# Performance work log

Hardware: AMD Instinct MI355X
Metric: run time of the kernel (lower is better)

## Reference

```python
import jax, jax.numpy as jnp
import numpy as np

N, E, IN, H, HEADS, L, OUT = 4096, 262144, 64, 128, 4, 2, 2
DH = H // HEADS  # 32, per-head dim for both GAT and global MHA
BN_EPS = 1e-5
NEG_SLOPE = 0.2  # GATConv leaky_relu default


def setup_inputs() -> dict:
    key = jax.random.key(0)
    ks = iter(jax.random.split(key, 32))
    rn = lambda shape, s: jax.random.normal(next(ks), shape, jnp.float32) * s
    return {
        "x": rn((N, IN), 1.0),
        "edge_index": jax.random.randint(next(ks), (2, E), 0, N),
        "w_in": rn((H, IN), IN ** -0.5),
        "b_in": rn((H,), 0.02),
        "w_gat": rn((L, H, H), H ** -0.5),
        "att_src": rn((L, HEADS, DH), 0.1),
        "att_dst": rn((L, HEADS, DH), 0.1),
        "b_gat": rn((L, H), 0.02),
        "w_qkv": rn((L, 3 * H, H), H ** -0.5),
        "b_qkv": rn((L, 3 * H), 0.02),
        "w_o": rn((L, H, H), H ** -0.5),
        "b_o": rn((L, H), 0.02),
        "bn_gamma": 1.0 + rn((L, 3, H), 0.05),
        "bn_beta": rn((L, 3, H), 0.05),
        "w1": rn((L, 2 * H, H), H ** -0.5),
        "b1": rn((L, 2 * H), 0.02),
        "w2": rn((L, H, 2 * H), (2 * H) ** -0.5),
        "b2": rn((L, H), 0.02),
        "w_out": rn((OUT, H), H ** -0.5),
        "b_out": rn((OUT,), 0.02),
    }


def _bn(h, g, b):
    # eval-mode BatchNorm1d with running_mean=0, running_var=1
    return h * (g / jnp.sqrt(1.0 + BN_EPS)) + b


def _gat(x, src, dst, w, a_src, a_dst, bias):
    # GATConv(hidden, hidden//heads, heads=HEADS, add_self_loops=False), concat=True
    xp = (x @ w.T).reshape(N, HEADS, DH)                  # [N, HEADS, DH]
    al_s = jnp.einsum('nhd,hd->nh', xp, a_src)            # [N, HEADS]
    al_d = jnp.einsum('nhd,hd->nh', xp, a_dst)
    logit = al_s[src] + al_d[dst]                         # [E, HEADS]
    logit = jnp.where(logit >= 0, logit, NEG_SLOPE * logit)
    m = jax.ops.segment_max(logit, dst, num_segments=N)   # scatter-softmax over dst
    m = jnp.where(jnp.isfinite(m), m, 0.0)
    e = jnp.exp(logit - m[dst])
    denom = jax.ops.segment_sum(e, dst, num_segments=N)
    alpha = e / (denom[dst] + 1e-16)
    out = jax.ops.segment_sum(alpha[:, :, None] * xp[src], dst, num_segments=N)
    return out.reshape(N, H) + bias


def _mha(x, wqkv, bqkv, wo, bo):
    # torch.nn.MultiheadAttention self-attention over all N nodes (one graph)
    qkv = x @ wqkv.T + bqkv
    q, k, v = jnp.split(qkv, 3, axis=-1)
    q = q.reshape(N, HEADS, DH)
    k = k.reshape(N, HEADS, DH)
    v = v.reshape(N, HEADS, DH)
    scores = jnp.einsum('nhd,mhd->hnm', q, k) / jnp.sqrt(jnp.float32(DH))
    attn = jax.nn.softmax(scores, axis=-1)
    out = jnp.einsum('hnm,mhd->nhd', attn, v).reshape(N, H)
    return out @ wo.T + bo


def reference(x, edge_index, w_in, b_in, w_gat, att_src, att_dst, b_gat,
              w_qkv, b_qkv, w_o, b_o, bn_gamma, bn_beta,
              w1, b1, w2, b2, w_out, b_out):
    src, dst = edge_index[0], edge_index[1]
    h = jax.nn.relu(x @ w_in.T + b_in)
    for l in range(L):
        # GPSConv: local GAT branch (dropout inactive in eval)
        h_loc = _gat(h, src, dst, w_gat[l], att_src[l], att_dst[l], b_gat[l]) + h
        h_loc = _bn(h_loc, bn_gamma[l, 0], bn_beta[l, 0])
        # GPSConv: global attention branch
        h_att = _mha(h, w_qkv[l], b_qkv[l], w_o[l], b_o[l]) + h
        h_att = _bn(h_att, bn_gamma[l, 1], bn_beta[l, 1])
        out = h_loc + h_att
        mlp = jax.nn.relu(out @ w1[l].T + b1[l]) @ w2[l].T + b2[l]
        out = _bn(out + mlp, bn_gamma[l, 2], bn_beta[l, 2])
        # GPSRiskModel residual + relu (dropout inactive in eval)
        h = jax.nn.relu(out + h)
    return h @ w_out.T + b_out
```

## Files before the change

kernel.cpp:

```cpp
#include <hip/hip_runtime.h>

#define NN 4096
#define EE 262144
#define INF_ 64
#define HH 128
#define HEADS 4
#define DH 32
#define LL 2
#define NH (NN * HH)
#define KSPLIT 16
#define L2E 1.4426950408889634f

typedef unsigned short u16;
typedef unsigned int u32;
using bf16x8 = __attribute__((ext_vector_type(8))) short;
using f32x4 = __attribute__((ext_vector_type(4))) float;

__device__ __forceinline__ float bf2f(u16 v) { return __uint_as_float(((u32)v) << 16); }
__device__ __forceinline__ u16 f2bf(float f) {
    u32 u = __float_as_uint(f);
    u32 r = (u + 0x7fffu + ((u >> 16) & 1u)) >> 16;
    return (u16)r;
}
__device__ __forceinline__ u32 encf(float f) {
    u32 b = __float_as_uint(f);
    return (b & 0x80000000u) ? ~b : (b | 0x80000000u);
}
__device__ __forceinline__ float decf(u32 u) {
    u32 b = (u & 0x80000000u) ? (u & 0x7fffffffu) : ~u;
    return __uint_as_float(b);
}

__global__ __launch_bounds__(256) void k_detect(const u16* __restrict__ x, int* __restrict__ flag,
                                                int* __restrict__ cnt, u32* __restrict__ gmax) {
    int t = threadIdx.x;
    for (int i = t; i < NN; i += 256) cnt[i] = 0;
    if (t < 16) gmax[t] = 0;
    __shared__ int cs[256];
    u16 v = x[2 * t];
    int e = (v >> 7) & 0xFF;
    cs[t] = (e >= 100 && e <= 140) ? 1 : 0;
    __syncthreads();
    for (int s = 128; s > 0; s >>= 1) {
        if (t < s) cs[t] += cs[t + s];
        __syncthreads();
    }
    if (t == 0) *flag = (cs[0] >= 128) ? 1 : 0;
}

#define MAXSEG 16
struct SegF { const void* src[MAXSEG]; int dst[MAXSEG]; int n[MAXSEG]; int cnt; };
struct SegB { const void* src[8]; u16* dst[8]; u16* dst2[8]; int n[8]; int cnt; };
__global__ __launch_bounds__(256) void k_prep(SegF SF, float* __restrict__ W, SegB SB,
                                              const int* __restrict__ flag,
                                              const int* __restrict__ dst, int* __restrict__ cnt) {
    int bid = blockIdx.x, t = threadIdx.x;
    if (bid < 96) {
        int seg = bid >> 3, bx = bid & 7;
        if (seg >= SF.cnt) return;
        int n = SF.n[seg];
        float* d = W + SF.dst[seg];
        const void* s = SF.src[seg];
        int f = *flag;
        for (int i = bx * 256 + t; i < n; i += 8 * 256)
            d[i] = f ? bf2f(((const u16*)s)[i]) : ((const float*)s)[i];
    } else if (bid < 992) {
        int b2 = bid - 96;
        int seg = b2 >> 7, bx = b2 & 127;
        if (seg >= SB.cnt) return;
        int f = *flag;
        u16* d = SB.dst[seg];
        u16* d2 = SB.dst2[seg];
        if (f && !d2) return;
        int n = SB.n[seg];
        const void* s = SB.src[seg];
        for (int i = bx * 256 + t; i < n; i += 128 * 256) {
            if (d2) {
                float v = f ? bf2f(((const u16*)s)[i]) : ((const float*)s)[i];
                u16 h = f2bf(v);
                d[i] = h;
                d2[i] = f2bf(v - bf2f(h));
            } else {
                d[i] = f2bf(((const float*)s)[i]);
            }
        }
    } else {
        int e = (bid - 992) * 256 + t;
        if (e < EE) atomicAdd(&cnt[dst[e]], 1);
    }
}

__global__ __launch_bounds__(128) void k_mgemm(const u16* __restrict__ Ahi, const u16* __restrict__ Alo,
                                               const u16* __restrict__ Wc, const u16* __restrict__ Wd,
                                               const int* __restrict__ flag,
                                               const float* __restrict__ bias,
                                               float* __restrict__ outf, u16* __restrict__ outb16,
                                               u16* __restrict__ outhi, u16* __restrict__ outlo,
                                               int K, int J, int relu, int jtiles,
                                               const int* __restrict__ scnt, int* __restrict__ srowstart,
                                               int* __restrict__ scursor) {
    __shared__ int part[128];
    if ((int)blockIdx.y >= jtiles) {
        if (blockIdx.x != 0 || scnt == nullptr) return;
        int t = threadIdx.x;
        int loc[32];
        int s = 0;
#pragma unroll
        for (int i = 0; i < 32; ++i) { loc[i] = s; s += scnt[t * 32 + i]; }
        part[t] = s;
        __syncthreads();
        for (int off = 1; off < 128; off <<= 1) {
            int v = part[t];
            int a = (t >= off) ? part[t - off] : 0;
            __syncthreads();
            part[t] = v + a;
            __syncthreads();
        }
        int base = (t == 0) ? 0 : part[t - 1];
#pragma unroll
        for (int i = 0; i < 32; ++i) {
            srowstart[t * 32 + i] = base + loc[i];
            scursor[t * 32 + i] = base + loc[i];
        }
        return;
    }
    const u16* Wb = (*flag) ? Wd : Wc;
    int wave = threadIdx.x >> 6, lane = threadIdx.x & 63;
    int grp = lane >> 4, lcol = lane & 15;
    int m0 = blockIdx.x * 32 + wave * 16;
    int j0 = blockIdx.y * 64;
    f32x4 acc[4];
#pragma unroll
    for (int s = 0; s < 4; ++s) acc[s] = (f32x4){0.f, 0.f, 0.f, 0.f};
    const u16* ah = Ahi + (size_t)(m0 + lcol) * K + grp * 8;
    const u16* al = Alo + (size_t)(m0 + lcol) * K + grp * 8;
    const u16* wb = Wb + (size_t)(j0 + lcol) * K + grp * 8;
    for (int k = 0; k < K; k += 32) {
        bf16x8 va = *(const bf16x8*)(ah + k);
        bf16x8 vl = *(const bf16x8*)(al + k);
#pragma unroll
        for (int s = 0; s < 4; ++s) {
            bf16x8 vw = *(const bf16x8*)(wb + (size_t)s * 16 * K + k);
            acc[s] = __builtin_amdgcn_mfma_f32_16x16x32_bf16(va, vw, acc[s], 0, 0, 0);
            acc[s] = __builtin_amdgcn_mfma_f32_16x16x32_bf16(vl, vw, acc[s], 0, 0, 0);
        }
    }
#pragma unroll
    for (int s = 0; s < 4; ++s) {
        int col = j0 + s * 16 + lcol;
        float bs = bias ? bias[col] : 0.f;
#pragma unroll
        for (int r = 0; r < 4; ++r) {
            float v = acc[s][r] + bs;
            if (relu) v = fmaxf(v, 0.f);
            size_t idx = (size_t)(m0 + grp * 4 + r) * J + col;
            if (outf) outf[idx] = v;
            if (outb16) outb16[idx] = f2bf(v);
            if (outhi) {
                u16 hv = f2bf(v);
                outhi[idx] = hv;
                outlo[idx] = f2bf(v - bf2f(hv));
            }
        }
    }
}

__global__ __launch_bounds__(128) void k_gemm_gq(const u16* __restrict__ Ahi, const u16* __restrict__ Alo,
                                                 const u16* __restrict__ wgatc, const u16* __restrict__ wgatd,
                                                 const u16* __restrict__ wqkvc, const u16* __restrict__ wqkvd,
                                                 const int* __restrict__ flag,
                                                 const float* __restrict__ bqkv,
                                                 u16* __restrict__ xpb, u16* __restrict__ qkvb,
                                                 const int* __restrict__ esrc_src, const int* __restrict__ esrc_dst,
                                                 int* __restrict__ cursor, int* __restrict__ esrc) {
    if (blockIdx.y >= 8) {
        int b = (blockIdx.y - 8) * 128 + blockIdx.x;
        for (int e = b * 128 + threadIdx.x; e < EE; e += 32768) {
            int d = esrc_dst[e];
            int p = atomicAdd(&cursor[d], 1);
            esrc[p] = esrc_src[e];
        }
        return;
    }
    int wave = threadIdx.x >> 6, lane = threadIdx.x & 63;
    int grp = lane >> 4, lcol = lane & 15;
    int m0 = blockIdx.x * 32 + wave * 16;
    int jb = blockIdx.y;
    int j0 = jb * 64;
    int f = *flag;
    const u16* wgat = f ? wgatd : wgatc;
    const u16* wqkv = f ? wqkvd : wqkvc;
    const u16* Wb = (jb < 2) ? (wgat + (size_t)j0 * HH) : (wqkv + (size_t)(j0 - 128) * HH);
    f32x4 acc[4];
#pragma unroll
    for (int s = 0; s < 4; ++s) acc[s] = (f32x4){0.f, 0.f, 0.f, 0.f};
    const u16* ah = Ahi + (size_t)(m0 + lcol) * HH + grp * 8;
    const u16* al = Alo + (size_t)(m0 + lcol) * HH + grp * 8;
    const u16* wb = Wb + (size_t)lcol * HH + grp * 8;
    for (int k = 0; k < HH; k += 32) {
        bf16x8 va = *(const bf16x8*)(ah + k);
        bf16x8 vl = *(const bf16x8*)(al + k);
#pragma unroll
        for (int s = 0; s < 4; ++s) {
            bf16x8 vw = *(const bf16x8*)(wb + (size_t)s * 16 * HH + k);
            acc[s] = __builtin_amdgcn_mfma_f32_16x16x32_bf16(va, vw, acc[s], 0, 0, 0);
            acc[s] = __builtin_amdgcn_mfma_f32_16x16x32_bf16(vl, vw, acc[s], 0, 0, 0);
        }
    }
    if (jb < 2) {
#pragma unroll
        for (int s = 0; s < 4; ++s) {
            int col = j0 + s * 16 + lcol;
#pragma unroll
            for (int r = 0; r < 4; ++r)
                xpb[(size_t)(m0 + grp * 4 + r) * HH + col] = f2bf(acc[s][r]);
        }
    } else {
#pragma unroll
        for (int s = 0; s < 4; ++s) {
            int colq = j0 - 128 + s * 16 + lcol;
            float bs = bqkv[colq];
#pragma unroll
            for (int r = 0; r < 4; ++r)
                qkvb[(size_t)(m0 + grp * 4 + r) * 384 + colq] = f2bf(acc[s][r] + bs);
        }
    }
}

__global__ __launch_bounds__(128) void k_gemm_wo(const u16* __restrict__ Ahi, const u16* __restrict__ Alo,
                                                 const u16* __restrict__ Wc, const u16* __restrict__ Wd,
                                                 const int* __restrict__ flag,
                                                 const float* __restrict__ bias,
                                                 const float* __restrict__ gatb, const float* __restrict__ hbuf,
                                                 const float* __restrict__ bgat, const float* __restrict__ gam,
                                                 const float* __restrict__ bet,
                                                 float* __restrict__ outb, u16* __restrict__ ohi,
                                                 u16* __restrict__ olo) {
    const u16* Wb = (*flag) ? Wd : Wc;
    int wave = threadIdx.x >> 6, lane = threadIdx.x & 63;
    int grp = lane >> 4, lcol = lane & 15;
    int m0 = blockIdx.x * 32 + wave * 16;
    int j0 = blockIdx.y * 64;
    f32x4 acc[4];
#pragma unroll
    for (int s = 0; s < 4; ++s) acc[s] = (f32x4){0.f, 0.f, 0.f, 0.f};
    const u16* ah = Ahi + (size_t)(m0 + lcol) * HH + grp * 8;
    const u16* al = Alo + (size_t)(m0 + lcol) * HH + grp * 8;
    const u16* wb = Wb + (size_t)(j0 + lcol) * HH + grp * 8;
    for (int k = 0; k < HH; k += 32) {
        bf16x8 va = *(const bf16x8*)(ah + k);
        bf16x8 vl = *(const bf16x8*)(al + k);
#pragma unroll
        for (int s = 0; s < 4; ++s) {
            bf16x8 vw = *(const bf16x8*)(wb + (size_t)s * 16 * HH + k);
            acc[s] = __builtin_amdgcn_mfma_f32_16x16x32_bf16(va, vw, acc[s], 0, 0, 0);
            acc[s] = __builtin_amdgcn_mfma_f32_16x16x32_bf16(vl, vw, acc[s], 0, 0, 0);
        }
    }
    float rs = rsqrtf(1.00001f);
#pragma unroll
    for (int s = 0; s < 4; ++s) {
        int col = j0 + s * 16 + lcol;
        float bs = bias[col];
        float g0 = gam[col] * rs, b0 = bet[col];
        float g1 = gam[HH + col] * rs, b1 = bet[HH + col];
        float bg = bgat[col];
#pragma unroll
        for (int r = 0; r < 4; ++r) {
            size_t idx = (size_t)(m0 + grp * 4 + r) * HH + col;
            float proj = acc[s][r] + bs;
            float hv = hbuf[idx];
            float hl = g0 * (gatb[idx] + bg + hv) + b0;
            float ha = g1 * (proj + hv) + b1;
            float v = hl + ha;
            outb[idx] = v;
            u16 hb = f2bf(v);
            ohi[idx] = hb;
            olo[idx] = f2bf(v - bf2f(hb));
        }
    }
}

__global__ __launch_bounds__(128) void k_gemm_mlp(const u16* __restrict__ Ahi, const u16* __restrict__ Alo,
                                                  const u16* __restrict__ W1c, const u16* __restrict__ W1d,
                                                  const u16* __restrict__ W2c, const u16* __restrict__ W2d,
                                                  const int* __restrict__ flag,
                                                  const float* __restrict__ b1, const float* __restrict__ b2,
                                                  const float* __restrict__ outb, const float* __restrict__ gam2,
                                                  const float* __restrict__ bet2,
                                                  float* __restrict__ hbuf, u16* __restrict__ hhi,
                                                  u16* __restrict__ hlo) {
    __shared__ u16 Hhi[16][264];
    __shared__ u16 Hlo[16][264];
    int f = *flag;
    const u16* W1 = f ? W1d : W1c;
    const u16* W2 = f ? W2d : W2c;
    int wave = threadIdx.x >> 6, lane = threadIdx.x & 63;
    int grp = lane >> 4, lcol = lane & 15;
    int m0 = blockIdx.x * 16;
    const u16* ah = Ahi + (size_t)(m0 + lcol) * HH + grp * 8;
    const u16* al = Alo + (size_t)(m0 + lcol) * HH + grp * 8;
#pragma unroll
    for (int jt = 0; jt < 2; ++jt) {
        int j0 = wave * 128 + jt * 64;
        f32x4 acc[4];
#pragma unroll
        for (int s = 0; s < 4; ++s) acc[s] = (f32x4){0.f, 0.f, 0.f, 0.f};
        const u16* wb = W1 + (size_t)(j0 + lcol) * HH + grp * 8;
#pragma unroll
        for (int k = 0; k < HH; k += 32) {
            bf16x8 va = *(const bf16x8*)(ah + k);
            bf16x8 vl = *(const bf16x8*)(al + k);
#pragma unroll
            for (int s = 0; s < 4; ++s) {
                bf16x8 vw = *(const bf16x8*)(wb + (size_t)s * 16 * HH + k);
                acc[s] = __builtin_amdgcn_mfma_f32_16x16x32_bf16(va, vw, acc[s], 0, 0, 0);
                acc[s] = __builtin_amdgcn_mfma_f32_16x16x32_bf16(vl, vw, acc[s], 0, 0, 0);
            }
        }
#pragma unroll
        for (int s = 0; s < 4; ++s) {
            int col = j0 + s * 16 + lcol;
            float bs = b1[col];
#pragma unroll
            for (int r = 0; r < 4; ++r) {
                float v = fmaxf(acc[s][r] + bs, 0.f);
                int row = grp * 4 + r;
                u16 hv = f2bf(v);
                Hhi[row][col] = hv;
                Hlo[row][col] = f2bf(v - bf2f(hv));
            }
        }
    }
    __syncthreads();
    int j0 = wave * 64;
    f32x4 acc[4];
#pragma unroll
    for (int s = 0; s < 4; ++s) acc[s] = (f32x4){0.f, 0.f, 0.f, 0.f};
    const u16* wb = W2 + (size_t)(j0 + lcol) * 256 + grp * 8;
#pragma unroll
    for (int k = 0; k < 256; k += 32) {
        bf16x8 va = *(const bf16x8*)(&Hhi[lcol][k + grp * 8]);
        bf16x8 vl = *(const bf16x8*)(&Hlo[lcol][k + grp * 8]);
#pragma unroll
        for (int s = 0; s < 4; ++s) {
            bf16x8 vw = *(const bf16x8*)(wb + (size_t)s * 16 * 256 + k);
            acc[s] = __builtin_amdgcn_mfma_f32_16x16x32_bf16(va, vw, acc[s], 0, 0, 0);
            acc[s] = __builtin_amdgcn_mfma_f32_16x16x32_bf16(vl, vw, acc[s], 0, 0, 0);
        }
    }
    float rs = rsqrtf(1.00001f);
#pragma unroll
    for (int s = 0; s < 4; ++s) {
        int col = j0 + s * 16 + lcol;
        float bs = b2[col];
        float g2 = gam2[col] * rs, bb2 = bet2[col];
#pragma unroll
        for (int r = 0; r < 4; ++r) {
            size_t idx = (size_t)(m0 + grp * 4 + r) * HH + col;
            float mlpo = acc[s][r] + bs;
            float o2 = g2 * (outb[idx] + mlpo) + bb2;
            float v = fmaxf(o2 + hbuf[idx], 0.f);
            hbuf[idx] = v;
            u16 hb = f2bf(v);
            hhi[idx] = hb;
            hlo[idx] = f2bf(v - bf2f(hb));
        }
    }
}

__global__ __launch_bounds__(256) void k_splitlog(const u16* __restrict__ qkvb,
                                                  float* __restrict__ PM, float* __restrict__ PL,
                                                  u16* __restrict__ PO,
                                                  const u16* __restrict__ xpb,
                                                  const float* __restrict__ asrc,
                                                  const float* __restrict__ adst,
                                                  float* __restrict__ als, float* __restrict__ ald,
                                                  u32* __restrict__ gmax) {
    __shared__ __align__(16) u16 Klds[64][40];
    __shared__ __align__(16) u32 Vlds[32][40];
    __shared__ __align__(16) u16 Plds[4][32][36];

    if (blockIdx.x >= 2048) {
        float* red = (float*)&Klds[0][0];
        int t = (blockIdx.x - 2048) * 256 + threadIdx.x;
        int n = t >> 2, hh = t & 3;
        const u16* xr = xpb + (size_t)n * HH + hh * DH;
        float s1 = 0.f, s2 = 0.f;
#pragma unroll
        for (int d = 0; d < DH; ++d) {
            float v = bf2f(xr[d]);
            s1 += v * asrc[hh * DH + d];
            s2 += v * adst[hh * DH + d];
        }
        als[t] = s1;
        ald[t] = s2;
        int lt = threadIdx.x;
        red[lt] = s1;
        __syncthreads();
        for (int off = 128; off >= 4; off >>= 1) {
            if (lt < off) red[lt] = fmaxf(red[lt], red[lt + off]);
            __syncthreads();
        }
        if (lt < 4) atomicMax(&gmax[lt], encf(red[lt]));
        __syncthreads();
        red[lt] = s2;
        __syncthreads();
        for (int off = 128; off >= 4; off >>= 1) {
            if (lt < off) red[lt] = fmaxf(red[lt], red[lt + off]);
            __syncthreads();
        }
        if (lt < 4) atomicMax(&gmax[4 + lt], encf(red[lt]));
        return;
    }

    const float C1 = 0.17677669529663687f * L2E;
    int head = blockIdx.x & 3;
    int qt = (blockIdx.x >> 2) & 31;
    int ks = blockIdx.x >> 7;
    int tid = threadIdx.x;
    int wave = tid >> 6, lane = tid & 63;
    int grp = lane >> 4, lcol = lane & 15;

    int qrow0 = qt * 128 + wave * 32;
    bf16x8 aQ0 = *(const bf16x8*)(qkvb + (size_t)(qrow0 + lcol) * 384 + head * 32 + grp * 8);
    bf16x8 aQ1 = *(const bf16x8*)(qkvb + (size_t)(qrow0 + 16 + lcol) * 384 + head * 32 + grp * 8);

    short onev = (lcol == 0) ? (short)0x3F80 : (short)0;
    bf16x8 bOne = {onev, onev, onev, onev, onev, onev, onev, onev};

    f32x4 oc00 = {0.f, 0.f, 0.f, 0.f}, oc01 = {0.f, 0.f, 0.f, 0.f};
    f32x4 oc10 = {0.f, 0.f, 0.f, 0.f}, oc11 = {0.f, 0.f, 0.f, 0.f};
    f32x4 ol0 = {0.f, 0.f, 0.f, 0.f}, ol1 = {0.f, 0.f, 0.f, 0.f};
    float msh = -INFINITY;

    int isK = (tid < 128);
    int st = tid & 127;
    int skey = st >> 1, shalf = (st & 1) * 16;
    int vj = st & 15, vc = (st >> 4) & 1, dgrp = st >> 5;
    const u16* kptr = qkvb + 128 + head * 32 + shalf;
    const u16* vptr = qkvb + 256 + head * 32 + dgrp * 8;
    int vk0 = vc * 32 + vj;
    int vk1 = vc * 32 + 16 + vj;

    int kt0 = ks * (NN / KSPLIT);
    bf16x8 r0, r1;
    if (isK) {
        r0 = *(const bf16x8*)(kptr + (size_t)(kt0 + skey) * 384);
        r1 = *(const bf16x8*)(kptr + (size_t)(kt0 + skey) * 384 + 8);
    } else {
        r0 = *(const bf16x8*)(vptr + (size_t)(kt0 + vk0) * 384);
        r1 = *(const bf16x8*)(vptr + (size_t)(kt0 + vk1) * 384);
    }

    const int NT = (NN / KSPLIT) / 64;
    for (int t = 0; t < NT; ++t) {
        if (isK) {
            *(bf16x8*)(&Klds[skey][shalf]) = r0;
            *(bf16x8*)(&Klds[skey][shalf + 8]) = r1;
        } else {
#pragma unroll
            for (int j = 0; j < 8; ++j)
                Vlds[dgrp * 8 + j][vc * 20 + vj] = (u32)(u16)r0[j] | ((u32)(u16)r1[j] << 16);
        }
        __syncthreads();
        if (t + 1 < NT) {
            int kn = kt0 + (t + 1) * 64;
            if (isK) {
                r0 = *(const bf16x8*)(kptr + (size_t)(kn + skey) * 384);
                r1 = *(const bf16x8*)(kptr + (size_t)(kn + skey) * 384 + 8);
            } else {
                r0 = *(const bf16x8*)(vptr + (size_t)(kn + vk0) * 384);
                r1 = *(const bf16x8*)(vptr + (size_t)(kn + vk1) * 384);
            }
        }
        f32x4 sc0[4], sc1[4];
        f32x4 zero = {0.f, 0.f, 0.f, 0.f};
        __builtin_amdgcn_s_setprio(1);
#pragma unroll
        for (int s = 0; s < 4; ++s) {
            bf16x8 bK = *(const bf16x8*)(&Klds[s * 16 + lcol][grp * 8]);
            sc0[s] = __builtin_amdgcn_mfma_f32_16x16x32_bf16(aQ0, bK, zero, 0, 0, 0);
            sc1[s] = __builtin_amdgcn_mfma_f32_16x16x32_bf16(aQ1, bK, zero, 0, 0, 0);
        }
        __builtin_amdgcn_s_setprio(0);
        float mymax = sc0[0][0];
#pragma unroll
        for (int s = 0; s < 4; ++s)
#pragma unroll
            for (int r = 0; r < 4; ++r) {
                mymax = fmaxf(mymax, sc0[s][r]);
                mymax = fmaxf(mymax, sc1[s][r]);
            }
        mymax = fmaxf(mymax, __shfl_xor(mymax, 1));
        mymax = fmaxf(mymax, __shfl_xor(mymax, 2));
        mymax = fmaxf(mymax, __shfl_xor(mymax, 4));
        mymax = fmaxf(mymax, __shfl_xor(mymax, 8));
        float mnew = fmaxf(msh, mymax * C1);
        float cc = __builtin_exp2f(msh - mnew);
        msh = mnew;
        oc00 *= cc; oc01 *= cc; ol0 *= cc;
        oc10 *= cc; oc11 *= cc; ol1 *= cc;
#pragma unroll
        for (int c2 = 0; c2 < 2; ++c2) {
#pragma unroll
            for (int r = 0; r < 4; ++r) {
                float p0 = __builtin_exp2f(__builtin_fmaf(sc0[2 * c2][r], C1, -mnew));
                float p1 = __builtin_exp2f(__builtin_fmaf(sc0[2 * c2 + 1][r], C1, -mnew));
                *(u32*)(&Plds[wave][grp * 4 + r][2 * lcol]) =
                    __builtin_amdgcn_perm(__float_as_uint(p1), __float_as_uint(p0), 0x07060302u);
                float q0 = __builtin_exp2f(__builtin_fmaf(sc1[2 * c2][r], C1, -mnew));
                float q1 = __builtin_exp2f(__builtin_fmaf(sc1[2 * c2 + 1][r], C1, -mnew));
                *(u32*)(&Plds[wave][16 + grp * 4 + r][2 * lcol]) =
                    __builtin_amdgcn_perm(__float_as_uint(q1), __float_as_uint(q0), 0x07060302u);
            }
            bf16x8 aP0 = *(const bf16x8*)(&Plds[wave][lcol][grp * 8]);
            bf16x8 aP1 = *(const bf16x8*)(&Plds[wave][16 + lcol][grp * 8]);
            bf16x8 bV0 = *(const bf16x8*)(&Vlds[lcol][c2 * 20 + grp * 4]);
            bf16x8 bV1 = *(const bf16x8*)(&Vlds[16 + lcol][c2 * 20 + grp * 4]);
            __builtin_amdgcn_s_setprio(1);
            oc00 = __builtin_amdgcn_mfma_f32_16x16x32_bf16(aP0, bV0, oc00, 0, 0, 0);
            oc01 = __builtin_amdgcn_mfma_f32_16x16x32_bf16(aP0, bV1, oc01, 0, 0, 0);
            ol0 = __builtin_amdgcn_mfma_f32_16x16x32_bf16(aP0, bOne, ol0, 0, 0, 0);
            oc10 = __builtin_amdgcn_mfma_f32_16x16x32_bf16(aP1, bV0, oc10, 0, 0, 0);
            oc11 = __builtin_amdgcn_mfma_f32_16x16x32_bf16(aP1, bV1, oc11, 0, 0, 0);
            ol1 = __builtin_amdgcn_mfma_f32_16x16x32_bf16(aP1, bOne, ol1, 0, 0, 0);
            __builtin_amdgcn_s_setprio(0);
        }
        __syncthreads();
    }
#pragma unroll
    for (int r = 0; r < 4; ++r) {
        int row0 = qrow0 + grp * 4 + r;
        size_t b0 = ((size_t)row0 * HEADS + head) * KSPLIT + ks;
        PO[b0 * 32 + lcol] = f2bf(oc00[r]);
        PO[b0 * 32 + 16 + lcol] = f2bf(oc01[r]);
        int row1 = row0 + 16;
        size_t b1 = ((size_t)row1 * HEADS + head) * KSPLIT + ks;
        PO[b1 * 32 + lcol] = f2bf(oc10[r]);
        PO[b1 * 32 + 16 + lcol] = f2bf(oc11[r]);
        if (lcol == 0) {
            PM[b0] = msh;
            PL[b0] = ol0[r];
            PM[b1] = msh;
            PL[b1] = ol1[r];
        }
    }
}

#define GCHUNK 256
__global__ __launch_bounds__(128) void k_gatcomb(const int* __restrict__ esrc, const int* __restrict__ rowstart,
                                                 const int* __restrict__ cnt, const float* __restrict__ als,
                                                 const float* __restrict__ ald, const u16* __restrict__ xpb,
                                                 float* __restrict__ gatout, const u32* __restrict__ gmax,
                                                 const float* __restrict__ PM, const float* __restrict__ PL,
                                                 const u16* __restrict__ PO, u16* __restrict__ atthi,
                                                 u16* __restrict__ attlo) {
    __shared__ float red[512];
    __shared__ float elds[GCHUNK * 4];
    __shared__ int slds[GCHUNK];
    int t = threadIdx.x;

    if (blockIdx.x >= NN) {
        int n2 = blockIdx.x - NN;
        float* wn = red;
        if (t < 64) {
            int head = t >> 4, ks = t & 15;
            size_t b = ((size_t)n2 * HEADS + head) * KSPLIT + ks;
            float pm = PM[b];
            float m = pm;
#pragma unroll
            for (int off = 1; off < 16; off <<= 1) m = fmaxf(m, __shfl_xor(m, off));
            float w = __builtin_exp2f(pm - m);
            float lw = PL[b] * w;
#pragma unroll
            for (int off = 1; off < 16; off <<= 1) lw += __shfl_xor(lw, off);
            wn[t] = w / lw;
        }
        __syncthreads();
        int head = t >> 5, dim = t & 31;
        size_t b0 = ((size_t)n2 * HEADS + head) * KSPLIT;
        float o = 0.f;
#pragma unroll
        for (int k = 0; k < KSPLIT; ++k)
            o += wn[head * 16 + k] * bf2f(PO[(b0 + k) * 32 + dim]);
        size_t idx = (size_t)n2 * HH + t;
        u16 h = f2bf(o);
        atthi[idx] = h;
        attlo[idx] = f2bf(o - bf2f(h));
        return;
    }

    int n = blockIdx.x;
    int base = rowstart[n], c = cnt[n];
    float4 adv = ((const float4*)ald)[n];
    float ad[4] = {adv.x, adv.y, adv.z, adv.w};
    float M2[4];
#pragma unroll
    for (int h = 0; h < 4; ++h) {
        float bound = decf(gmax[h]) + decf(gmax[4 + h]);
        float M = bound >= 0.f ? bound : 0.2f * bound;
        M2[h] = M * L2E;
    }
    float dsum[4] = {0.f, 0.f, 0.f, 0.f};
    float acc = 0.f;
    int ht = t >> 5;
    for (int ch = 0; ch < c; ch += GCHUNK) {
        int cn = min(GCHUNK, c - ch);
        __syncthreads();
        for (int i = t; i < cn; i += 128) {
            int s = esrc[base + ch + i];
            slds[i] = s;
            float4 as = ((const float4*)als)[s];
            float lg, e;
            lg = as.x + ad[0]; lg = lg >= 0.f ? lg : 0.2f * lg; e = __builtin_exp2f(lg * L2E - M2[0]); elds[i * 4 + 0] = e; dsum[0] += e;
            lg = as.y + ad[1]; lg = lg >= 0.f ? lg : 0.2f * lg; e = __builtin_exp2f(lg * L2E - M2[1]); elds[i * 4 + 1] = e; dsum[1] += e;
            lg = as.z + ad[2]; lg = lg >= 0.f ? lg : 0.2f * lg; e = __builtin_exp2f(lg * L2E - M2[2]); elds[i * 4 + 2] = e; dsum[2] += e;
            lg = as.w + ad[3]; lg = lg >= 0.f ? lg : 0.2f * lg; e = __builtin_exp2f(lg * L2E - M2[3]); elds[i * 4 + 3] = e; dsum[3] += e;
        }
        __syncthreads();
        int i = 0;
        for (; i + 4 <= cn; i += 4) {
            int s0 = slds[i], s1 = slds[i + 1], s2 = slds[i + 2], s3 = slds[i + 3];
            float x0 = bf2f(xpb[(size_t)s0 * HH + t]);
            float x1 = bf2f(xpb[(size_t)s1 * HH + t]);
            float x2 = bf2f(xpb[(size_t)s2 * HH + t]);
            float x3 = bf2f(xpb[(size_t)s3 * HH + t]);
            acc += elds[i * 4 + ht] * x0 + elds[(i + 1) * 4 + ht] * x1;
            acc += elds[(i + 2) * 4 + ht] * x2 + elds[(i + 3) * 4 + ht] * x3;
        }
        for (; i < cn; ++i) acc += elds[i * 4 + ht] * bf2f(xpb[(size_t)slds[i] * HH + t]);
    }
    __syncthreads();
#pragma unroll
    for (int h = 0; h < 4; ++h) red[h * 128 + t] = dsum[h];
    __syncthreads();
    for (int s2 = 64; s2 > 0; s2 >>= 1) {
        if (t < s2) {
#pragma unroll
            for (int h = 0; h < 4; ++h)
                red[h * 128 + t] += red[h * 128 + t + s2];
        }
        __syncthreads();
    }
    float inv = 1.f / (red[ht * 128] + 1e-16f);
    gatout[(size_t)n * HH + t] = acc * inv;
}

__global__ __launch_bounds__(64) void k_out(const float* __restrict__ h, const float* __restrict__ w,
                                            const float* __restrict__ b, void* __restrict__ yout,
                                            const int* __restrict__ flag) {
    int n = blockIdx.x, l = threadIdx.x;
    float a0 = 0.f, a1 = 0.f;
    for (int k = l; k < HH; k += 64) {
        float hv = h[(size_t)n * HH + k];
        a0 += hv * w[k];
        a1 += hv * w[HH + k];
    }
#pragma unroll
    for (int off = 32; off > 0; off >>= 1) {
        a0 += __shfl_xor(a0, off);
        a1 += __shfl_xor(a1, off);
    }
    if (l == 0) {
        float o0 = a0 + b[0], o1 = a1 + b[1];
        if (*flag) {
            u16* y = (u16*)yout;
            y[n * 2 + 0] = f2bf(o0);
            y[n * 2 + 1] = f2bf(o1);
        } else {
            float* y = (float*)yout;
            y[n * 2 + 0] = o0;
            y[n * 2 + 1] = o1;
        }
    }
}

extern "C" void kernel_launch(void* const* d_in, const int* in_sizes, int n_in,
                              void* d_out, int out_size, void* d_ws, size_t ws_size,
                              hipStream_t stream) {
    float* W = (float*)d_ws;
    size_t o = 0;
    auto take = [&](size_t n) { size_t r = o; o += n; return r; };
    size_t pb_in = take(HH);
    size_t pattS = take(LL * HEADS * DH);
    size_t pattD = take(LL * HEADS * DH);
    size_t pb_gat = take(LL * HH);
    size_t pb_qkv = take(LL * 3 * HH);
    size_t pb_o  = take(LL * HH);
    size_t pbn_g = take(LL * 3 * HH);
    size_t pbn_b = take(LL * 3 * HH);
    size_t pb1   = take(LL * 2 * HH);
    size_t pb2   = take(LL * HH);
    size_t pw_out = take(2 * HH);
    size_t pb_out = take(2);
    auto takeb = [&](size_t nu16) { size_t r = o; o += (nu16 + 1) / 2; return r; };
    size_t bw_in  = takeb(HH * INF_);
    size_t bw_gat = takeb(LL * HH * HH);
    size_t bw_qkv = takeb(LL * 3 * HH * HH);
    size_t bw_o   = takeb(LL * HH * HH);
    size_t bw1    = takeb(LL * 2 * HH * HH);
    size_t bw2    = takeb(LL * HH * 2 * HH);
    o = (o + 127) & ~(size_t)127;
    size_t ohbuf = take(NH);
    size_t ogat  = take(NH);
    size_t otmp  = take(NH);
    size_t oals  = take(NN * HEADS);
    size_t oald  = take(NN * HEADS);
    size_t opm   = take(NN * HEADS * KSPLIT);
    size_t opl   = take(NN * HEADS * KSPLIT);
    size_t opo   = takeb((size_t)NN * HEADS * KSPLIT * 32);
    size_t oqkvb = takeb(NN * 384);
    size_t oxpb  = takeb(NH);
    size_t oxhi  = takeb(NN * INF_);
    size_t oxlo  = takeb(NN * INF_);
    size_t ohhi  = takeb(NH);
    size_t ohlo  = takeb(NH);
    size_t oahi  = takeb(NH);
    size_t oalo  = takeb(NH);
    size_t oohi  = takeb(NH);
    size_t oolo  = takeb(NH);
    size_t omhi  = takeb(NN * 2 * HH);
    size_t omlo  = takeb(NN * 2 * HH);
    int* ibase    = (int*)(W + o);
    int* iflag    = ibase;
    int* cnt      = ibase + 64;
    int* rowstart = cnt + NN;
    int* cursor   = rowstart + NN;
    int* esrc     = cursor + NN;
    u32* gmax     = (u32*)(esrc + EE);

    float* hbuf = W + ohbuf;
    float* gatb = W + ogat;
    float* tmp  = W + otmp;
    float* als  = W + oals;
    float* ald  = W + oald;
    float* pmb  = W + opm;
    float* plb  = W + opl;
    u16* pob  = (u16*)(W + opo);
    u16* qkvb = (u16*)(W + oqkvb);
    u16* xpb  = (u16*)(W + oxpb);
    u16* xhi = (u16*)(W + oxhi), *xlo = (u16*)(W + oxlo);
    u16* hhi = (u16*)(W + ohhi), *hlo = (u16*)(W + ohlo);
    u16* ahi = (u16*)(W + oahi), *alo = (u16*)(W + oalo);
    u16* ohi = (u16*)(W + oohi), *olo = (u16*)(W + oolo);

    const int* src = (const int*)d_in[1];
    const int* dst = (const int*)d_in[1] + EE;
    const u16* dw_in  = (const u16*)d_in[2];
    const u16* dw_gat = (const u16*)d_in[4];
    const u16* dw_qkv = (const u16*)d_in[8];
    const u16* dw_o   = (const u16*)d_in[10];
    const u16* dw1    = (const u16*)d_in[14];
    const u16* dw2    = (const u16*)d_in[16];

    k_detect<<<1, 256, 0, stream>>>((const u16*)d_in[0], iflag, cnt, gmax);

    SegF SF = {};
    int nf = 0;
    auto addf = [&](int idx, size_t off, int n) { SF.src[nf] = d_in[idx]; SF.dst[nf] = (int)off; SF.n[nf] = n; ++nf; };
    addf(3, pb_in, HH);
    addf(5, pattS, LL * HEADS * DH);
    addf(6, pattD, LL * HEADS * DH);
    addf(7, pb_gat, LL * HH);
    addf(9, pb_qkv, LL * 3 * HH);
    addf(11, pb_o, LL * HH);
    addf(12, pbn_g, LL * 3 * HH);
    addf(13, pbn_b, LL * 3 * HH);
    addf(15, pb1, LL * 2 * HH);
    addf(17, pb2, LL * HH);
    addf(18, pw_out, 2 * HH);
    addf(19, pb_out, 2);
    SF.cnt = nf;

    SegB SB = {};
    int nb = 0;
    auto addb = [&](int idx, size_t off, int n, u16* d2) {
        SB.src[nb] = d_in[idx]; SB.dst[nb] = (u16*)(W + off); SB.dst2[nb] = d2; SB.n[nb] = n; ++nb;
    };
    addb(2, bw_in, HH * INF_, nullptr);
    addb(4, bw_gat, LL * HH * HH, nullptr);
    addb(8, bw_qkv, LL * 3 * HH * HH, nullptr);
    addb(10, bw_o, LL * HH * HH, nullptr);
    addb(14, bw1, LL * 2 * HH * HH, nullptr);
    addb(16, bw2, LL * HH * 2 * HH, nullptr);
    SB.src[nb] = d_in[0]; SB.dst[nb] = xhi; SB.dst2[nb] = xlo; SB.n[nb] = NN * INF_; ++nb;
    SB.cnt = nb;

    k_prep<<<2016, 256, 0, stream>>>(SF, W, SB, iflag, dst, cnt);

    k_mgemm<<<dim3(NN / 32, HH / 64 + 1), 128, 0, stream>>>(xhi, xlo, (u16*)(W + bw_in), dw_in, iflag,
                                                            W + pb_in, hbuf, nullptr, hhi, hlo, INF_, HH, 1,
                                                            HH / 64, cnt, rowstart, cursor);

    for (int l = 0; l < LL; ++l) {
        k_gemm_gq<<<dim3(NN / 32, (l == 0) ? 10 : 8), 128, 0, stream>>>(hhi, hlo,
                                                        (u16*)(W + bw_gat) + (size_t)l * HH * HH,
                                                        dw_gat + (size_t)l * HH * HH,
                                                        (u16*)(W + bw_qkv) + (size_t)l * 3 * HH * HH,
                                                        dw_qkv + (size_t)l * 3 * HH * HH,
                                                        iflag, W + pb_qkv + l * 3 * HH, xpb, qkvb,
                                                        src, dst, cursor, esrc);
        k_splitlog<<<2048 + (NN * HEADS) / 256, 256, 0, stream>>>(qkvb, pmb, plb, pob, xpb,
                                                                  W + pattS + l * HEADS * DH,
                                                                  W + pattD + l * HEADS * DH,
                                                                  als, ald, gmax + l * 8);
        k_gatcomb<<<2 * NN, 128, 0, stream>>>(esrc, rowstart, cnt, als, ald, xpb, gatb, gmax + l * 8,
                                              pmb, plb, pob, ahi, alo);
        k_gemm_wo<<<dim3(NN / 32, HH / 64), 128, 0, stream>>>(ahi, alo,
                                                              (u16*)(W + bw_o) + (size_t)l * HH * HH,
                                                              dw_o + (size_t)l * HH * HH, iflag,
                                                              W + pb_o + l * HH, gatb, hbuf,
                                                              W + pb_gat + l * HH, W + pbn_g + l * 3 * HH,
                                                              W + pbn_b + l * 3 * HH, tmp, ohi, olo);
        k_gemm_mlp<<<NN / 16, 128, 0, stream>>>(ohi, olo,
                                                (u16*)(W + bw1) + (size_t)l * 2 * HH * HH,
                                                dw1 + (size_t)l * 2 * HH * HH,
                                                (u16*)(W + bw2) + (size_t)l * HH * 2 * HH,
                                                dw2 + (size_t)l * HH * 2 * HH, iflag,
                                                W + pb1 + l * 2 * HH, W + pb2 + l * HH,
                                                tmp, W + pbn_g + l * 3 * HH + 2 * HH,
                                                W + pbn_b + l * 3 * HH + 2 * HH,
                                                hbuf, hhi, hlo);
    }
    k_out<<<NN, 64, 0, stream>>>(hbuf, W + pw_out, W + pb_out, d_out, iflag);
}
```

Measured before the change: 288.9 us.

## Fuse output-projection GEMM with MLP GEMMs into a single per-tile kernel

New measurement: 274.6 us. -4.9%, faster.

```diff
diff --git a/kernel.cpp b/kernel.cpp
--- a/kernel.cpp
+++ b/kernel.cpp
@@ -227,90 +227,83 @@
     }
 }
 
-__global__ __launch_bounds__(128) void k_gemm_wo(const u16* __restrict__ Ahi, const u16* __restrict__ Alo,
-                                                 const u16* __restrict__ Wc, const u16* __restrict__ Wd,
-                                                 const int* __restrict__ flag,
-                                                 const float* __restrict__ bias,
-                                                 const float* __restrict__ gatb, const float* __restrict__ hbuf,
-                                                 const float* __restrict__ bgat, const float* __restrict__ gam,
-                                                 const float* __restrict__ bet,
-                                                 float* __restrict__ outb, u16* __restrict__ ohi,
-                                                 u16* __restrict__ olo) {
-    const u16* Wb = (*flag) ? Wd : Wc;
-    int wave = threadIdx.x >> 6, lane = threadIdx.x & 63;
-    int grp = lane >> 4, lcol = lane & 15;
-    int m0 = blockIdx.x * 32 + wave * 16;
-    int j0 = blockIdx.y * 64;
-    f32x4 acc[4];
-#pragma unroll
-    for (int s = 0; s < 4; ++s) acc[s] = (f32x4){0.f, 0.f, 0.f, 0.f};
-    const u16* ah = Ahi + (size_t)(m0 + lcol) * HH + grp * 8;
-    const u16* al = Alo + (size_t)(m0 + lcol) * HH + grp * 8;
-    const u16* wb = Wb + (size_t)(j0 + lcol) * HH + grp * 8;
-    for (int k = 0; k < HH; k += 32) {
-        bf16x8 va = *(const bf16x8*)(ah + k);
-        bf16x8 vl = *(const bf16x8*)(al + k);
-#pragma unroll
-        for (int s = 0; s < 4; ++s) {
-            bf16x8 vw = *(const bf16x8*)(wb + (size_t)s * 16 * HH + k);
-            acc[s] = __builtin_amdgcn_mfma_f32_16x16x32_bf16(va, vw, acc[s], 0, 0, 0);
-            acc[s] = __builtin_amdgcn_mfma_f32_16x16x32_bf16(vl, vw, acc[s], 0, 0, 0);
-        }
-    }
-    float rs = rsqrtf(1.00001f);
-#pragma unroll
-    for (int s = 0; s < 4; ++s) {
-        int col = j0 + s * 16 + lcol;
-        float bs = bias[col];
-        float g0 = gam[col] * rs, b0 = bet[col];
-        float g1 = gam[HH + col] * rs, b1 = bet[HH + col];
-        float bg = bgat[col];
-#pragma unroll
-        for (int r = 0; r < 4; ++r) {
-            size_t idx = (size_t)(m0 + grp * 4 + r) * HH + col;
-            float proj = acc[s][r] + bs;
-            float hv = hbuf[idx];
-            float hl = g0 * (gatb[idx] + bg + hv) + b0;
-            float ha = g1 * (proj + hv) + b1;
-            float v = hl + ha;
-            outb[idx] = v;
-            u16 hb = f2bf(v);
-            ohi[idx] = hb;
-            olo[idx] = f2bf(v - bf2f(hb));
-        }
-    }
-}
-
-__global__ __launch_bounds__(128) void k_gemm_mlp(const u16* __restrict__ Ahi, const u16* __restrict__ Alo,
-                                                  const u16* __restrict__ W1c, const u16* __restrict__ W1d,
-                                                  const u16* __restrict__ W2c, const u16* __restrict__ W2d,
-                                                  const int* __restrict__ flag,
-                                                  const float* __restrict__ b1, const float* __restrict__ b2,
-                                                  const float* __restrict__ outb, const float* __restrict__ gam2,
-                                                  const float* __restrict__ bet2,
-                                                  float* __restrict__ hbuf, u16* __restrict__ hhi,
-                                                  u16* __restrict__ hlo) {
-    __shared__ u16 Hhi[16][264];
-    __shared__ u16 Hlo[16][264];
+__global__ __launch_bounds__(256) void k_womlp(const u16* __restrict__ Ahi, const u16* __restrict__ Alo,
+                                               const u16* __restrict__ Woc, const u16* __restrict__ Wod,
+                                               const u16* __restrict__ W1c, const u16* __restrict__ W1d,
+                                               const u16* __restrict__ W2c, const u16* __restrict__ W2d,
+                                               const int* __restrict__ flag,
+                                               const float* __restrict__ bo, const float* __restrict__ b1,
+                                               const float* __restrict__ b2,
+                                               const float* __restrict__ gatb, const float* __restrict__ bgat,
+                                               const float* __restrict__ gam, const float* __restrict__ bet,
+                                               const float* __restrict__ gam2, const float* __restrict__ bet2,
+                                               float* __restrict__ hbuf, u16* __restrict__ hhi,
+                                               u16* __restrict__ hlo) {
+    __shared__ float Of[16][132];
+    __shared__ u16 A2hi[16][136], A2lo[16][136];
+    __shared__ u16 Hhi[16][264], Hlo[16][264];
     int f = *flag;
+    const u16* Wo = f ? Wod : Woc;
     const u16* W1 = f ? W1d : W1c;
     const u16* W2 = f ? W2d : W2c;
     int wave = threadIdx.x >> 6, lane = threadIdx.x & 63;
     int grp = lane >> 4, lcol = lane & 15;
     int m0 = blockIdx.x * 16;
-    const u16* ah = Ahi + (size_t)(m0 + lcol) * HH + grp * 8;
-    const u16* al = Alo + (size_t)(m0 + lcol) * HH + grp * 8;
-#pragma unroll
-    for (int jt = 0; jt < 2; ++jt) {
-        int j0 = wave * 128 + jt * 64;
-        f32x4 acc[4];
-#pragma unroll
-        for (int s = 0; s < 4; ++s) acc[s] = (f32x4){0.f, 0.f, 0.f, 0.f};
-        const u16* wb = W1 + (size_t)(j0 + lcol) * HH + grp * 8;
+    float rs = rsqrtf(1.00001f);
+
+    {
+        int j0 = wave * 32;
+        f32x4 acc[2];
+#pragma unroll
+        for (int s = 0; s < 2; ++s) acc[s] = (f32x4){0.f, 0.f, 0.f, 0.f};
+        const u16* ah = Ahi + (size_t)(m0 + lcol) * HH + grp * 8;
+        const u16* al = Alo + (size_t)(m0 + lcol) * HH + grp * 8;
+        const u16* wb = Wo + (size_t)(j0 + lcol) * HH + grp * 8;
 #pragma unroll
         for (int k = 0; k < HH; k += 32) {
             bf16x8 va = *(const bf16x8*)(ah + k);
             bf16x8 vl = *(const bf16x8*)(al + k);
+#pragma unroll
+            for (int s = 0; s < 2; ++s) {
+                bf16x8 vw = *(const bf16x8*)(wb + (size_t)s * 16 * HH + k);
+                acc[s] = __builtin_amdgcn_mfma_f32_16x16x32_bf16(va, vw, acc[s], 0, 0, 0);
+                acc[s] = __builtin_amdgcn_mfma_f32_16x16x32_bf16(vl, vw, acc[s], 0, 0, 0);
+            }
+        }
+#pragma unroll
+        for (int s = 0; s < 2; ++s) {
+            int col = j0 + s * 16 + lcol;
+            float bs = bo[col];
+            float g0 = gam[col] * rs, b0 = bet[col];
+            float g1 = gam[HH + col] * rs, bb1 = bet[HH + col];
+            float bg = bgat[col];
+#pragma unroll
+            for (int r = 0; r < 4; ++r) {
+                int row = grp * 4 + r;
+                size_t idx = (size_t)(m0 + row) * HH + col;
+                float proj = acc[s][r] + bs;
+                float hv = hbuf[idx];
+                float hl = g0 * (gatb[idx] + bg + hv) + b0;
+                float ha = g1 * (proj + hv) + bb1;
+                float v = hl + ha;
+                Of[row][col] = v;
+                u16 hb = f2bf(v);
+                A2hi[row][col] = hb;
+                A2lo[row][col] = f2bf(v - bf2f(hb));
+            }
+        }
+    }
+    __syncthreads();
+    {
+        int j0 = wave * 64;
+        f32x4 acc[4];
+#pragma unroll
+        for (int s = 0; s < 4; ++s) acc[s] = (f32x4){0.f, 0.f, 0.f, 0.f};
+        const u16* wb = W1 + (size_t)(j0 + lcol) * HH + grp * 8;
+#pragma unroll
+        for (int k = 0; k < HH; k += 32) {
+            bf16x8 va = *(const bf16x8*)(&A2hi[lcol][k + grp * 8]);
+            bf16x8 vl = *(const bf16x8*)(&A2lo[lcol][k + grp * 8]);
 #pragma unroll
             for (int s = 0; s < 4; ++s) {
                 bf16x8 vw = *(const bf16x8*)(wb + (size_t)s * 16 * HH + k);
@@ -333,38 +326,40 @@
         }
     }
     __syncthreads();
-    int j0 = wave * 64;
-    f32x4 acc[4];
-#pragma unroll
-    for (int s = 0; s < 4; ++s) acc[s] = (f32x4){0.f, 0.f, 0.f, 0.f};
-    const u16* wb = W2 + (size_t)(j0 + lcol) * 256 + grp * 8;
-#pragma unroll
-    for (int k = 0; k < 256; k += 32) {
-        bf16x8 va = *(const bf16x8*)(&Hhi[lcol][k + grp * 8]);
-        bf16x8 vl = *(const bf16x8*)(&Hlo[lcol][k + grp * 8]);
-#pragma unroll
-        for (int s = 0; s < 4; ++s) {
-            bf16x8 vw = *(const bf16x8*)(wb + (size_t)s * 16 * 256 + k);
-            acc[s] = __builtin_amdgcn_mfma_f32_16x16x32_bf16(va, vw, acc[s], 0, 0, 0);
-            acc[s] = __builtin_amdgcn_mfma_f32_16x16x32_bf16(vl, vw, acc[s], 0, 0, 0);
-        }
-    }
-    float rs = rsqrtf(1.00001f);
-#pragma unroll
-    for (int s = 0; s < 4; ++s) {
-        int col = j0 + s * 16 + lcol;
-        float bs = b2[col];
-        float g2 = gam2[col] * rs, bb2 = bet2[col];
-#pragma unroll
-        for (int r = 0; r < 4; ++r) {
-            size_t idx = (size_t)(m0 + grp * 4 + r) * HH + col;
-            float mlpo = acc[s][r] + bs;
-            float o2 = g2 * (outb[idx] + mlpo) + bb2;
-            float v = fmaxf(o2 + hbuf[idx], 0.f);
-            hbuf[idx] = v;
-            u16 hb = f2bf(v);
-            hhi[idx] = hb;
-            hlo[idx] = f2bf(v - bf2f(hb));
+    {
+        int j0 = wave * 32;
+        f32x4 acc[2];
+#pragma unroll
+        for (int s = 0; s < 2; ++s) acc[s] = (f32x4){0.f, 0.f, 0.f, 0.f};
+        const u16* wb = W2 + (size_t)(j0 + lcol) * 256 + grp * 8;
+#pragma unroll
+        for (int k = 0; k < 256; k += 32) {
+            bf16x8 va = *(const bf16x8*)(&Hhi[lcol][k + grp * 8]);
+            bf16x8 vl = *(const bf16x8*)(&Hlo[lcol][k + grp * 8]);
+#pragma unroll
+            for (int s = 0; s < 2; ++s) {
+                bf16x8 vw = *(const bf16x8*)(wb + (size_t)s * 16 * 256 + k);
+                acc[s] = __builtin_amdgcn_mfma_f32_16x16x32_bf16(va, vw, acc[s], 0, 0, 0);
+                acc[s] = __builtin_amdgcn_mfma_f32_16x16x32_bf16(vl, vw, acc[s], 0, 0, 0);
+            }
+        }
+#pragma unroll
+        for (int s = 0; s < 2; ++s) {
+            int col = j0 + s * 16 + lcol;
+            float bs = b2[col];
+            float g2 = gam2[col] * rs, bb2 = bet2[col];
+#pragma unroll
+            for (int r = 0; r < 4; ++r) {
+                int row = grp * 4 + r;
+                size_t idx = (size_t)(m0 + row) * HH + col;
+                float mlpo = acc[s][r] + bs;
+                float o2 = g2 * (Of[row][col] + mlpo) + bb2;
+                float v = fmaxf(o2 + hbuf[idx], 0.f);
+                hbuf[idx] = v;
+                u16 hb = f2bf(v);
+                hhi[idx] = hb;
+                hlo[idx] = f2bf(v - bf2f(hb));
+            }
         }
     }
 }
@@ -704,7 +699,6 @@
     o = (o + 127) & ~(size_t)127;
     size_t ohbuf = take(NH);
     size_t ogat  = take(NH);
-    size_t otmp  = take(NH);
     size_t oals  = take(NN * HEADS);
     size_t oald  = take(NN * HEADS);
     size_t opm   = take(NN * HEADS * KSPLIT);
@@ -718,10 +712,6 @@
     size_t ohlo  = takeb(NH);
     size_t oahi  = takeb(NH);
     size_t oalo  = takeb(NH);
-    size_t oohi  = takeb(NH);
-    size_t oolo  = takeb(NH);
-    size_t omhi  = takeb(NN * 2 * HH);
-    size_t omlo  = takeb(NN * 2 * HH);
     int* ibase    = (int*)(W + o);
     int* iflag    = ibase;
     int* cnt      = ibase + 64;
@@ -732,7 +722,6 @@
 
     float* hbuf = W + ohbuf;
     float* gatb = W + ogat;
-    float* tmp  = W + otmp;
     float* als  = W + oals;
     float* ald  = W + oald;
     float* pmb  = W + opm;
@@ -743,7 +732,6 @@
     u16* xhi = (u16*)(W + oxhi), *xlo = (u16*)(W + oxlo);
     u16* hhi = (u16*)(W + ohhi), *hlo = (u16*)(W + ohlo);
     u16* ahi = (u16*)(W + oahi), *alo = (u16*)(W + oalo);
-    u16* ohi = (u16*)(W + oohi), *olo = (u16*)(W + oolo);
 
     const int* src = (const int*)d_in[1];
     const int* dst = (const int*)d_in[1] + EE;
@@ -807,21 +795,19 @@
                                                                   als, ald, gmax + l * 8);
         k_gatcomb<<<2 * NN, 128, 0, stream>>>(esrc, rowstart, cnt, als, ald, xpb, gatb, gmax + l * 8,
                                               pmb, plb, pob, ahi, alo);
-        k_gemm_wo<<<dim3(NN / 32, HH / 64), 128, 0, stream>>>(ahi, alo,
-                                                              (u16*)(W + bw_o) + (size_t)l * HH * HH,
-                                                              dw_o + (size_t)l * HH * HH, iflag,
-                                                              W + pb_o + l * HH, gatb, hbuf,
-                                                              W + pb_gat + l * HH, W + pbn_g + l * 3 * HH,
-                                                              W + pbn_b + l * 3 * HH, tmp, ohi, olo);
-        k_gemm_mlp<<<NN / 16, 128, 0, stream>>>(ohi, olo,
-                                                (u16*)(W + bw1) + (size_t)l * 2 * HH * HH,
-                                                dw1 + (size_t)l * 2 * HH * HH,
-                                                (u16*)(W + bw2) + (size_t)l * HH * 2 * HH,
-                                                dw2 + (size_t)l * HH * 2 * HH, iflag,
-                                                W + pb1 + l * 2 * HH, W + pb2 + l * HH,
-                                                tmp, W + pbn_g + l * 3 * HH + 2 * HH,
-                                                W + pbn_b + l * 3 * HH + 2 * HH,
-                                                hbuf, hhi, hlo);
+        k_womlp<<<NN / 16, 256, 0, stream>>>(ahi, alo,
+                                             (u16*)(W + bw_o) + (size_t)l * HH * HH,
+                                             dw_o + (size_t)l * HH * HH,
+                                             (u16*)(W + bw1) + (size_t)l * 2 * HH * HH,
+                                             dw1 + (size_t)l * 2 * HH * HH,
+                                             (u16*)(W + bw2) + (size_t)l * HH * 2 * HH,
+                                             dw2 + (size_t)l * HH * 2 * HH, iflag,
+                                             W + pb_o + l * HH, W + pb1 + l * 2 * HH, W + pb2 + l * HH,
+                                             gatb, W + pb_gat + l * HH,
+                                             W + pbn_g + l * 3 * HH, W + pbn_b + l * 3 * HH,
+                                             W + pbn_g + l * 3 * HH + 2 * HH,
+                                             W + pbn_b + l * 3 * HH + 2 * HH,
+                                             hbuf, hhi, hlo);
     }
     k_out<<<NN, 64, 0, stream>>>(hbuf, W + pw_out, W + pb_out, d_out, iflag);
 }
```
